# Performance work log

Measured on AMD Instinct MI355X. Metric: run time of the kernel, lower is better.

## Reference

```python
import jax, jax.numpy as jnp
from jax import lax
import numpy as np

NUM_SUBCNNS = 3      # num_classes - 1
C_FEAT = 1024        # backbone feature channels (hard-coded in CAM loop)
STRIDE = 32          # 224 -> 7 spatial reduction, like densenet121 features


def setup_inputs() -> dict:
    key = jax.random.key(0)
    ks = jax.random.split(key, 8)
    B, H, W = 32, 224, 224
    x = jax.random.normal(ks[0], (B, 3, H, W), dtype=jnp.float32)
    # Stand-in backbone per branch: conv 3->1024, kernel=stride=32 (same output
    # shape/dataflow as densenet121 features: [B,1024,7,7]).
    Wb = jax.random.normal(ks[1], (NUM_SUBCNNS, C_FEAT, 3, STRIDE, STRIDE), dtype=jnp.float32) * 0.02
    bb = jnp.zeros((NUM_SUBCNNS, C_FEAT), dtype=jnp.float32)
    # projection head: Linear(1024,512) -> ReLU -> (Dropout, eval=identity) -> Linear(512,2)
    p1_w = jax.random.normal(ks[2], (NUM_SUBCNNS, 512, C_FEAT), dtype=jnp.float32) * 0.02
    p1_b = jnp.zeros((NUM_SUBCNNS, 512), dtype=jnp.float32)
    p2_w = jax.random.normal(ks[3], (NUM_SUBCNNS, 2, 512), dtype=jnp.float32) * 0.02
    p2_b = jnp.zeros((NUM_SUBCNNS, 2), dtype=jnp.float32)
    # classifier Linear(1024,2): only its weight is used, for the CAM reduction
    cls_w = jax.random.normal(ks[4], (NUM_SUBCNNS, 2, C_FEAT), dtype=jnp.float32) * 0.02
    return {"x": x, "Wb": Wb, "bb": bb, "p1_w": p1_w, "p1_b": p1_b,
            "p2_w": p2_w, "p2_b": p2_b, "cls_w": cls_w}


def reference(x, Wb, bb, p1_w, p1_b, p2_w, p2_b, cls_w):
    ranking_outputs = []
    cam_outputs = []
    features_list = []
    for i in range(NUM_SUBCNNS):
        # backbone feature extraction: [B,3,224,224] -> [B,1024,7,7]
        feats = lax.conv_general_dilated(
            x, Wb[i], window_strides=(STRIDE, STRIDE), padding="VALID",
            dimension_numbers=("NCHW", "OIHW", "NCHW")) + bb[i][None, :, None, None]
        features_list.append(feats)
        # global average pool over H,W
        pooled = jnp.mean(feats, axis=(2, 3))                       # [B,1024]
        # projection MLP (dropout is identity at inference)
        h = jax.nn.relu(pooled @ p1_w[i].T + p1_b[i])               # [B,512]
        logits = h @ p2_w[i].T + p2_b[i]                            # [B,2]
        ranking_outputs.append(jax.nn.softmax(logits, axis=1)[:, 1:2])  # [B,1]
        # CAM: the torch double python-loop == one contraction over channels
        cam = jax.nn.relu(jnp.einsum("oc,bchw->obhw", cls_w[i], feats))  # [2,B,7,7]
        cam_outputs.append((cam[0], cam[1]))
    ranking = jnp.concatenate(ranking_outputs, axis=1)              # [B,3]
    return ranking, cam_outputs, features_list
```

## Files before the change

### kernel.cpp

```cpp
#include <hip/hip_runtime.h>
#include <hip/hip_bf16.h>
#include <math.h>

#define NSUB   3
#define CFEAT  1024
#define KDIM   3072
#define MDIM   1568
#define BATCH  32
#define NMT    25
#define NKT    96

#define OUT_CAM   96
#define OUT_FEAT  9504
#define FEAT_PER_BRANCH (BATCH * CFEAT * 49)

#define WS_A      0
#define WS_W      (9600 * 1024)
#define WS_POOLED (WS_W + 18432 * 1024)
#define WS_H      (WS_POOLED + NSUB * BATCH * CFEAT * 4)
#define WS_CAMP   (WS_H + NSUB * BATCH * 512 * 4)

typedef __attribute__((ext_vector_type(8))) short bf16x8;
typedef __attribute__((ext_vector_type(4))) float f32x4;

__device__ __forceinline__ short b16(float f){
    __hip_bfloat16 h = __float2bfloat16(f);
    return *reinterpret_cast<short*>(&h);
}
__device__ __forceinline__ bf16x8 pack8(float4 a, float4 b){
    bf16x8 r;
    r[0]=b16(a.x); r[1]=b16(a.y); r[2]=b16(a.z); r[3]=b16(a.w);
    r[4]=b16(b.x); r[5]=b16(b.y); r[6]=b16(b.z); r[7]=b16(b.w);
    return r;
}

__global__ __launch_bounds__(256) void prep_frag(
    const float* __restrict__ x, const float* __restrict__ w,
    bf16x8* __restrict__ Af, bf16x8* __restrict__ Wf)
{
    int bid = blockIdx.x, t = threadIdx.x;
    if (bid < 4608) {
        int g = bid * 256 + t;
        int chunk = g >> 6, l = g & 63;
        int ni = chunk & 3, KT = (chunk >> 2) % 96, NTg = chunk / 384;
        int n = NTg * 64 + ni * 16 + (l & 15);
        int k = KT * 32 + (l >> 4) * 8;
        const float* src = w + (size_t)n * KDIM + k;
        Wf[(size_t)chunk * 64 + l] = pack8(*(const float4*)src, *(const float4*)(src + 4));
    } else {
        int g = (bid - 4608) * 256 + t;
        int chunk = g >> 6, l = g & 63;
        int mi = chunk & 3, KT = (chunk >> 2) % 96, MT = chunk / 384;
        int m  = MT * 64 + mi * 16 + (l & 15);
        int k0 = KT * 32 + (l >> 4) * 8;
        bf16x8 v;
        if (m < MDIM) {
            int b = m / 49, p = m % 49, ph = p / 7, pw = p % 7;
            int ch = k0 >> 10, r = (k0 >> 5) & 31, s = k0 & 31;
            const float* src = x + (((size_t)(b*3 + ch)*224 + ph*32 + r)*224 + pw*32 + s);
            v = pack8(*(const float4*)src, *(const float4*)(src + 4));
        } else {
            v = (bf16x8){0,0,0,0,0,0,0,0};
        }
        Af[(size_t)chunk * 64 + l] = v;
    }
}

__global__ __launch_bounds__(128) void conv_mfma(
    const bf16x8* __restrict__ Af, const bf16x8* __restrict__ Wf,
    const float* __restrict__ bb, float* __restrict__ out)
{
    int bid = (int)blockIdx.x;
    bid = (bid & 7) * 75 + (bid >> 3);
    const int i   = bid / 200;
    const int rem = bid % 200;
    const int NTb = rem / 25, MT = rem % 25;

    const int wv = threadIdx.x >> 6, l = threadIdx.x & 63;
    const int NT = NTb + wv * 8;
    const int lrow = l & 15, q = l >> 4;

    const bf16x8* Ab = Af + (size_t)(MT * 384) * 64 + l;
    const bf16x8* Bb = Wf + (size_t)((i*16 + NT) * 384) * 64 + l;

    f32x4 acc[4][4] = {};
    bf16x8 fa0[4], fb0[4], fa1[4], fb1[4];

#pragma unroll
    for (int m = 0; m < 4; ++m) { fa0[m] = Ab[m*64]; fb0[m] = Bb[m*64]; }

    for (int KT = 0; KT < NKT; KT += 2) {
        {
            const bf16x8* An = Ab + (KT + 1) * 256;
            const bf16x8* Bn = Bb + (KT + 1) * 256;
#pragma unroll
            for (int m = 0; m < 4; ++m) { fa1[m] = An[m*64]; fb1[m] = Bn[m*64]; }
        }
#pragma unroll
        for (int mi = 0; mi < 4; ++mi)
#pragma unroll
            for (int ni = 0; ni < 4; ++ni)
                acc[mi][ni] = __builtin_amdgcn_mfma_f32_16x16x32_bf16(
                    fa0[mi], fb0[ni], acc[mi][ni], 0, 0, 0);
        if (KT + 2 < NKT) {
            const bf16x8* An = Ab + (KT + 2) * 256;
            const bf16x8* Bn = Bb + (KT + 2) * 256;
#pragma unroll
            for (int m = 0; m < 4; ++m) { fa0[m] = An[m*64]; fb0[m] = Bn[m*64]; }
        }
#pragma unroll
        for (int mi = 0; mi < 4; ++mi)
#pragma unroll
            for (int ni = 0; ni < 4; ++ni)
                acc[mi][ni] = __builtin_amdgcn_mfma_f32_16x16x32_bf16(
                    fa1[mi], fb1[ni], acc[mi][ni], 0, 0, 0);
    }

    float* featb = out + OUT_FEAT + (size_t)i * FEAT_PER_BRANCH;
    float bias[4];
#pragma unroll
    for (int ni = 0; ni < 4; ++ni)
        bias[ni] = bb[i*CFEAT + NT*64 + ni*16 + lrow];
#pragma unroll
    for (int mi = 0; mi < 4; ++mi) {
        int mbase = MT*64 + mi*16 + q*4;
#pragma unroll
        for (int rr = 0; rr < 4; ++rr) {
            int m = mbase + rr;
            if (m >= MDIM) continue;
            int b = m / 49, p = m % 49;
#pragma unroll
            for (int ni = 0; ni < 4; ++ni) {
                int n = NT*64 + ni*16 + lrow;
                featb[(size_t)(b*CFEAT + n)*49 + p] = acc[mi][ni][rr] + bias[ni];
            }
        }
    }
}

__global__ __launch_bounds__(128) void cam_pool(
    const float* __restrict__ feat, const float* __restrict__ cls_w,
    float* __restrict__ pooled, float* __restrict__ camp)
{
    __shared__ float fs[128][50];
    int bid = blockIdx.x;
    int i = bid >> 8, b = (bid >> 3) & 31, ch = bid & 7;
    int t = threadIdx.x;
    int c0 = ch * 128;
    const float* f = feat + ((size_t)(i*BATCH + b) * CFEAT + c0) * 49;

    for (int qq = 0; qq < 49; ++qq) {
        int e = qq*128 + t;
        fs[e / 49][e % 49] = f[e];
    }
    __syncthreads();

    {
        float s = 0.f;
#pragma unroll
        for (int k = 0; k < 49; ++k) s += fs[t][k];
        pooled[(size_t)(i*BATCH + b) * CFEAT + c0 + t] = s * (1.f/49.f);
    }

    if (t < 98) {
        int o = t / 49, p = t % 49;
        const float* w = cls_w + (size_t)i * 2 * CFEAT + o * CFEAT + c0;
        float s = 0.f;
        for (int c = 0; c < 128; ++c) s += w[c] * fs[c][p];
        camp[(size_t)bid * 98 + t] = s;
    }
}

__global__ __launch_bounds__(256) void mlp1_kernel(
    const float* __restrict__ pooled, const float* __restrict__ p1w,
    const float* __restrict__ p1b, float* __restrict__ h,
    const float* __restrict__ camp, float* __restrict__ out_cam)
{
    if (blockIdx.x >= 48) {
        int fid = (blockIdx.x - 48) * 256 + threadIdx.x;
        if (fid < NSUB * 2 * MDIM) {
            int io = fid / MDIM, rem = fid % MDIM;
            int b = rem / 49, p = rem % 49;
            int i = io >> 1, o = io & 1;
            float s = 0.f;
#pragma unroll
            for (int c = 0; c < 8; ++c)
                s += camp[(size_t)(((i*BATCH + b)*8) + c) * 98 + o*49 + p];
            out_cam[fid] = fmaxf(s, 0.f);
        }
        return;
    }
    __shared__ float ps[32 * 256];
    int i = blockIdx.x >> 4, jc = blockIdx.x & 15;
    int t = threadIdx.x;
    int j = jc*32 + (t & 31);
    int bg = (t >> 5) * 4;
    float acc[4] = {};
    const float* wrow = p1w + ((size_t)i*512 + j) * CFEAT;
    for (int kc = 0; kc < 4; ++kc) {
        __syncthreads();
#pragma unroll
        for (int qq = 0; qq < 8; ++qq) {
            int f4 = t + qq*256;
            int b = f4 >> 6, k4 = (f4 & 63) * 4;
            *(float4*)&ps[b*256 + k4] =
                *(const float4*)&pooled[((size_t)i*32 + b)*CFEAT + kc*256 + k4];
        }
        __syncthreads();
        const float* wk = wrow + kc*256;
        for (int k = 0; k < 256; k += 4) {
            float4 w4 = *(const float4*)(wk + k);
#pragma unroll
            for (int qq = 0; qq < 4; ++qq) {
                const float* pr = &ps[(bg + qq)*256 + k];
                acc[qq] += w4.x*pr[0] + w4.y*pr[1] + w4.z*pr[2] + w4.w*pr[3];
            }
        }
    }
    float bias = p1b[i*512 + j];
#pragma unroll
    for (int qq = 0; qq < 4; ++qq)
        h[((size_t)i*32 + bg + qq)*512 + j] = fmaxf(acc[qq] + bias, 0.f);
}

__global__ void mlp2_kernel(const float* __restrict__ h, const float* __restrict__ p2w,
                            const float* __restrict__ p2b, float* __restrict__ out)
{
    __shared__ float part[256];
    int i = blockIdx.x, t = threadIdx.x;
    int b = t & 31, kc = t >> 5;
    const float* hv = h + ((size_t)i*32 + b)*512 + kc*64;
    const float* w0 = p2w + (size_t)i*1024 + kc*64;
    const float* w1 = w0 + 512;
    float s = 0.f;
    for (int k = 0; k < 64; ++k) s += hv[k] * (w1[k] - w0[k]);
    part[t] = s;
    __syncthreads();
    if (t < 32) {
        float d = 0.f;
#pragma unroll
        for (int qq = 0; qq < 8; ++qq) d += part[qq*32 + t];
        d += p2b[i*2 + 1] - p2b[i*2 + 0];
        out[b*NSUB + i] = 1.f / (1.f + expf(-d));
    }
}

extern "C" void kernel_launch(void* const* d_in, const int* in_sizes, int n_in,
                              void* d_out, int out_size, void* d_ws, size_t ws_size,
                              hipStream_t stream)
{
    const float* x    = (const float*)d_in[0];
    const float* Wb   = (const float*)d_in[1];
    const float* bbp  = (const float*)d_in[2];
    const float* p1w  = (const float*)d_in[3];
    const float* p1b  = (const float*)d_in[4];
    const float* p2w  = (const float*)d_in[5];
    const float* p2b  = (const float*)d_in[6];
    const float* clsw = (const float*)d_in[7];
    float* out = (float*)d_out;

    char* ws = (char*)d_ws;
    bf16x8* Af    = (bf16x8*)(ws + WS_A);
    bf16x8* Wf    = (bf16x8*)(ws + WS_W);
    float* pooled = (float*)(ws + WS_POOLED);
    float* hbuf   = (float*)(ws + WS_H);
    float* camp   = (float*)(ws + WS_CAMP);

    prep_frag<<<4608 + 2400, 256, 0, stream>>>(x, Wb, Af, Wf);
    conv_mfma<<<600, 128, 0, stream>>>(Af, Wf, bbp, out);
    cam_pool<<<NSUB*BATCH*8, 128, 0, stream>>>(out + OUT_FEAT, clsw, pooled, camp);
    mlp1_kernel<<<48 + 37, 256, 0, stream>>>(pooled, p1w, p1b, hbuf, camp, out + OUT_CAM);
    mlp2_kernel<<<NSUB, 256, 0, stream>>>(hbuf, p2w, p2b, out);
}
```

Before: 122.0 us.

## Triple-buffer MFMA operand loads and stage conv epilogue through LDS

Replaces the two-deep register prefetch in the conv GEMM with a three-stage rotation (loads for k-tile kt+2 are issued before the MFMAs for kt), so more global loads are in flight while the matrix cores work. The epilogue now writes each wave's 64x64 accumulator tile into padded shared memory and then stores it with each lane owning one spatial row, so consecutive lanes write adjacent feature elements instead of scattering across channels. It also adds a min-blocks-per-SM launch bound of 2. The extra register buffers and about 33KB of LDS per block may limit occupancy, and since each wave only touches its own LDS slice no barrier is needed.

```diff
diff --git a/kernel.cpp b/kernel.cpp
--- a/kernel.cpp
+++ b/kernel.cpp
@@ -66,10 +66,12 @@
     }
 }
 
-__global__ __launch_bounds__(128) void conv_mfma(
+__global__ __launch_bounds__(128, 2) void conv_mfma(
     const bf16x8* __restrict__ Af, const bf16x8* __restrict__ Wf,
     const float* __restrict__ bb, float* __restrict__ out)
 {
+    __shared__ float eplds[2][64 * 65];
+
     int bid = (int)blockIdx.x;
     bid = (bid & 7) * 75 + (bid >> 3);
     const int i   = bid / 200;
@@ -84,57 +86,55 @@
     const bf16x8* Bb = Wf + (size_t)((i*16 + NT) * 384) * 64 + l;
 
     f32x4 acc[4][4] = {};
-    bf16x8 fa0[4], fb0[4], fa1[4], fb1[4];
-
-#pragma unroll
-    for (int m = 0; m < 4; ++m) { fa0[m] = Ab[m*64]; fb0[m] = Bb[m*64]; }
-
-    for (int KT = 0; KT < NKT; KT += 2) {
-        {
-            const bf16x8* An = Ab + (KT + 1) * 256;
-            const bf16x8* Bn = Bb + (KT + 1) * 256;
-#pragma unroll
-            for (int m = 0; m < 4; ++m) { fa1[m] = An[m*64]; fb1[m] = Bn[m*64]; }
-        }
+    bf16x8 a0[4], b0[4], a1[4], b1[4], a2[4], b2[4];
+
+    auto LOADT = [&](bf16x8 (&Ad)[4], bf16x8 (&Bd)[4], int KT){
+        const bf16x8* An = Ab + KT * 256;
+        const bf16x8* Bn = Bb + KT * 256;
+#pragma unroll
+        for (int m2 = 0; m2 < 4; ++m2) { Ad[m2] = An[m2*64]; Bd[m2] = Bn[m2*64]; }
+    };
+    auto MFMAT = [&](bf16x8 (&As)[4], bf16x8 (&Bs)[4]){
 #pragma unroll
         for (int mi = 0; mi < 4; ++mi)
 #pragma unroll
             for (int ni = 0; ni < 4; ++ni)
                 acc[mi][ni] = __builtin_amdgcn_mfma_f32_16x16x32_bf16(
-                    fa0[mi], fb0[ni], acc[mi][ni], 0, 0, 0);
-        if (KT + 2 < NKT) {
-            const bf16x8* An = Ab + (KT + 2) * 256;
-            const bf16x8* Bn = Bb + (KT + 2) * 256;
-#pragma unroll
-            for (int m = 0; m < 4; ++m) { fa0[m] = An[m*64]; fb0[m] = Bn[m*64]; }
-        }
-#pragma unroll
-        for (int mi = 0; mi < 4; ++mi)
-#pragma unroll
-            for (int ni = 0; ni < 4; ++ni)
-                acc[mi][ni] = __builtin_amdgcn_mfma_f32_16x16x32_bf16(
-                    fa1[mi], fb1[ni], acc[mi][ni], 0, 0, 0);
-    }
-
-    float* featb = out + OUT_FEAT + (size_t)i * FEAT_PER_BRANCH;
+                    As[mi], Bs[ni], acc[mi][ni], 0, 0, 0);
+    };
+
+    LOADT(a0, b0, 0);
+    LOADT(a1, b1, 1);
+    for (int kt = 0; kt < NKT; kt += 3) {
+        LOADT(a2, b2, kt + 2);
+        MFMAT(a0, b0);
+        if (kt + 3 < NKT) LOADT(a0, b0, kt + 3);
+        MFMAT(a1, b1);
+        if (kt + 4 < NKT) LOADT(a1, b1, kt + 4);
+        MFMAT(a2, b2);
+    }
+
     float bias[4];
 #pragma unroll
     for (int ni = 0; ni < 4; ++ni)
         bias[ni] = bb[i*CFEAT + NT*64 + ni*16 + lrow];
-#pragma unroll
-    for (int mi = 0; mi < 4; ++mi) {
-        int mbase = MT*64 + mi*16 + q*4;
-#pragma unroll
-        for (int rr = 0; rr < 4; ++rr) {
-            int m = mbase + rr;
-            if (m >= MDIM) continue;
-            int b = m / 49, p = m % 49;
-#pragma unroll
-            for (int ni = 0; ni < 4; ++ni) {
-                int n = NT*64 + ni*16 + lrow;
-                featb[(size_t)(b*CFEAT + n)*49 + p] = acc[mi][ni][rr] + bias[ni];
-            }
-        }
+    float* ep = eplds[wv];
+#pragma unroll
+    for (int mi = 0; mi < 4; ++mi)
+#pragma unroll
+        for (int ni = 0; ni < 4; ++ni)
+#pragma unroll
+            for (int rr = 0; rr < 4; ++rr)
+                ep[(mi*16 + q*4 + rr) * 65 + ni*16 + lrow] = acc[mi][ni][rr] + bias[ni];
+
+    float* featb = out + OUT_FEAT + (size_t)i * FEAT_PER_BRANCH;
+    int m = MT*64 + l;
+    if (m < MDIM) {
+        int b = m / 49, p = m % 49;
+        float* base = featb + (size_t)(b*CFEAT + NT*64) * 49 + p;
+#pragma unroll 8
+        for (int c = 0; c < 64; ++c)
+            base[c * 49] = ep[l*65 + c];
     }
 }
 
```

Result: faster. 109.6 us (-10.2%).

## Stage A tiles through double-buffered LDS with 128x64 block tiles in conv GEMM

Applied to the files above, without the earlier changes.

The conv GEMM now uses 256-thread blocks, each computing a 128x64 output tile with four waves arranged 2x2. A fragments are loaded straight into double-buffered LDS with global_load_lds, so the waves sharing an A tile read it once instead of each reading it from global memory. B fragments are prefetched into registers one step ahead, and the MFMA sections run at raised wave priority. This cuts redundant global loads of A, at the cost of block-wide barriers, extra LDS traffic and one padded M tile that reads past the A buffer into unused rows.

```diff
diff --git a/kernel.cpp b/kernel.cpp
--- a/kernel.cpp
+++ b/kernel.cpp
@@ -7,8 +7,7 @@
 #define KDIM   3072
 #define MDIM   1568
 #define BATCH  32
-#define NMT    25
-#define NKT    96
+#define NK     48
 
 #define OUT_CAM   96
 #define OUT_FEAT  9504
@@ -32,6 +31,12 @@
     r[0]=b16(a.x); r[1]=b16(a.y); r[2]=b16(a.z); r[3]=b16(a.w);
     r[4]=b16(b.x); r[5]=b16(b.y); r[6]=b16(b.z); r[7]=b16(b.w);
     return r;
+}
+
+typedef const __attribute__((address_space(1))) void* gas1_t;
+typedef __attribute__((address_space(3))) void* las3_t;
+__device__ __forceinline__ void gl_lds16(const short* g, char* l){
+    __builtin_amdgcn_global_load_lds((gas1_t)g, (las3_t)l, 16, 0, 0);
 }
 
 __global__ __launch_bounds__(256) void prep_frag(
@@ -66,73 +71,112 @@
     }
 }
 
-__global__ __launch_bounds__(128) void conv_mfma(
+__global__ __launch_bounds__(256, 3) void conv_mfma(
     const bf16x8* __restrict__ Af, const bf16x8* __restrict__ Wf,
     const float* __restrict__ bb, float* __restrict__ out)
 {
+    __shared__ __align__(16) char lds[32768];
+
     int bid = (int)blockIdx.x;
-    bid = (bid & 7) * 75 + (bid >> 3);
-    const int i   = bid / 200;
-    const int rem = bid % 200;
-    const int NTb = rem / 25, MT = rem % 25;
-
-    const int wv = threadIdx.x >> 6, l = threadIdx.x & 63;
-    const int NT = NTb + wv * 8;
-    const int lrow = l & 15, q = l >> 4;
-
-    const bf16x8* Ab = Af + (size_t)(MT * 384) * 64 + l;
-    const bf16x8* Bb = Wf + (size_t)((i*16 + NT) * 384) * 64 + l;
-
-    f32x4 acc[4][4] = {};
-    bf16x8 fa0[4], fb0[4], fa1[4], fb1[4];
-
-#pragma unroll
-    for (int m = 0; m < 4; ++m) { fa0[m] = Ab[m*64]; fb0[m] = Bb[m*64]; }
-
-    for (int KT = 0; KT < NKT; KT += 2) {
-        {
-            const bf16x8* An = Ab + (KT + 1) * 256;
-            const bf16x8* Bn = Bb + (KT + 1) * 256;
-#pragma unroll
-            for (int m = 0; m < 4; ++m) { fa1[m] = An[m*64]; fb1[m] = Bn[m*64]; }
-        }
-#pragma unroll
-        for (int mi = 0; mi < 4; ++mi)
-#pragma unroll
-            for (int ni = 0; ni < 4; ++ni)
-                acc[mi][ni] = __builtin_amdgcn_mfma_f32_16x16x32_bf16(
-                    fa0[mi], fb0[ni], acc[mi][ni], 0, 0, 0);
-        if (KT + 2 < NKT) {
-            const bf16x8* An = Ab + (KT + 2) * 256;
-            const bf16x8* Bn = Bb + (KT + 2) * 256;
-#pragma unroll
-            for (int m = 0; m < 4; ++m) { fa0[m] = An[m*64]; fb0[m] = Bn[m*64]; }
-        }
-#pragma unroll
-        for (int mi = 0; mi < 4; ++mi)
-#pragma unroll
-            for (int ni = 0; ni < 4; ++ni)
-                acc[mi][ni] = __builtin_amdgcn_mfma_f32_16x16x32_bf16(
-                    fa1[mi], fb1[ni], acc[mi][ni], 0, 0, 0);
+    bid = (bid & 7) * 78 + (bid >> 3);
+    const int i   = bid / 208;
+    const int rem = bid % 208;
+    const int nt  = rem / 13, mt = rem % 13;
+
+    const int t = threadIdx.x, wv = t >> 6, l = t & 63;
+    const int wr = wv >> 1, wc = wv & 1;
+    const int lrow = l & 15, lsl = l >> 4;
+
+    const bf16x8* Ag[4]; int Ad[4];
+#pragma unroll
+    for (int q = 0; q < 4; ++q) {
+        int chunk = (2*mt + (wv >> 1))*384 + (wv & 1)*4 + q;
+        Ag[q] = Af + (size_t)chunk * 64 + l;
+        Ad[q] = (wv*4 + q) * 1024;
+    }
+
+    const int NTg = i*16 + nt;
+    const bf16x8* Bp[2][2];
+#pragma unroll
+    for (int ni = 0; ni < 2; ++ni)
+#pragma unroll
+        for (int kk = 0; kk < 2; ++kk)
+            Bp[ni][kk] = Wf + (size_t)(NTg*384 + kk*4 + wc*2 + ni) * 64 + l;
+
+    f32x4 acc[4][2] = {};
+    bf16x8 bgA[2][2], bgB[2][2];
+
+#pragma unroll
+    for (int q = 0; q < 4; ++q) gl_lds16((const short*)Ag[q], lds + Ad[q]);
+#pragma unroll
+    for (int ni = 0; ni < 2; ++ni)
+#pragma unroll
+        for (int kk = 0; kk < 2; ++kk)
+            bgA[ni][kk] = *Bp[ni][kk];
+
+    auto COMPUTE = [&](const char* base, bf16x8 (&BG)[2][2]) {
+        bf16x8 af[4][2];
+#pragma unroll
+        for (int kk = 0; kk < 2; ++kk)
+#pragma unroll
+            for (int mi = 0; mi < 4; ++mi)
+                af[mi][kk] = *(const bf16x8*)(base + ((wr*2 + kk)*4 + mi)*1024 + l*16);
+        __builtin_amdgcn_s_setprio(1);
+#pragma unroll
+        for (int kk = 0; kk < 2; ++kk)
+#pragma unroll
+            for (int mi = 0; mi < 4; ++mi)
+#pragma unroll
+                for (int ni = 0; ni < 2; ++ni)
+                    acc[mi][ni] = __builtin_amdgcn_mfma_f32_16x16x32_bf16(
+                        af[mi][kk], BG[ni][kk], acc[mi][ni], 0, 0, 0);
+        __builtin_amdgcn_s_setprio(0);
+    };
+
+    for (int kt = 0; kt < NK; kt += 2) {
+        __syncthreads();
+        if (kt + 1 < NK) {
+#pragma unroll
+            for (int q = 0; q < 4; ++q)
+                gl_lds16((const short*)(Ag[q] + (kt+1)*512), lds + 16384 + Ad[q]);
+#pragma unroll
+            for (int ni = 0; ni < 2; ++ni)
+#pragma unroll
+                for (int kk = 0; kk < 2; ++kk)
+                    bgB[ni][kk] = Bp[ni][kk][(size_t)(kt+1)*512];
+        }
+        COMPUTE(lds, bgA);
+        __syncthreads();
+        if (kt + 2 < NK) {
+#pragma unroll
+            for (int q = 0; q < 4; ++q)
+                gl_lds16((const short*)(Ag[q] + (kt+2)*512), lds + Ad[q]);
+#pragma unroll
+            for (int ni = 0; ni < 2; ++ni)
+#pragma unroll
+                for (int kk = 0; kk < 2; ++kk)
+                    bgA[ni][kk] = Bp[ni][kk][(size_t)(kt+2)*512];
+        }
+        COMPUTE(lds + 16384, bgB);
     }
 
     float* featb = out + OUT_FEAT + (size_t)i * FEAT_PER_BRANCH;
-    float bias[4];
-#pragma unroll
-    for (int ni = 0; ni < 4; ++ni)
-        bias[ni] = bb[i*CFEAT + NT*64 + ni*16 + lrow];
+    float bias[2];
+#pragma unroll
+    for (int ni = 0; ni < 2; ++ni)
+        bias[ni] = bb[i*CFEAT + nt*64 + wc*32 + ni*16 + lrow];
 #pragma unroll
     for (int mi = 0; mi < 4; ++mi) {
-        int mbase = MT*64 + mi*16 + q*4;
-#pragma unroll
-        for (int rr = 0; rr < 4; ++rr) {
-            int m = mbase + rr;
+        int mbase = mt*128 + wr*64 + mi*16 + lsl*4;
+#pragma unroll
+        for (int r = 0; r < 4; ++r) {
+            int m = mbase + r;
             if (m >= MDIM) continue;
-            int b = m / 49, p = m % 49;
-#pragma unroll
-            for (int ni = 0; ni < 4; ++ni) {
-                int n = NT*64 + ni*16 + lrow;
-                featb[(size_t)(b*CFEAT + n)*49 + p] = acc[mi][ni][rr] + bias[ni];
+            int b = m/49, p = m%49;
+#pragma unroll
+            for (int ni = 0; ni < 2; ++ni) {
+                int n = nt*64 + wc*32 + ni*16 + lrow;
+                featb[(size_t)(b*CFEAT + n)*49 + p] = acc[mi][ni][r] + bias[ni];
             }
         }
     }
@@ -267,7 +311,7 @@
     float* camp   = (float*)(ws + WS_CAMP);
 
     prep_frag<<<4608 + 2400, 256, 0, stream>>>(x, Wb, Af, Wf);
-    conv_mfma<<<600, 128, 0, stream>>>(Af, Wf, bbp, out);
+    conv_mfma<<<624, 256, 0, stream>>>(Af, Wf, bbp, out);
     cam_pool<<<NSUB*BATCH*8, 128, 0, stream>>>(out + OUT_FEAT, clsw, pooled, camp);
     mlp1_kernel<<<48 + 37, 256, 0, stream>>>(pooled, p1w, p1b, hbuf, camp, out + OUT_CAM);
     mlp2_kernel<<<NSUB, 256, 0, stream>>>(hbuf, p2w, p2b, out);
```

New measurement: 117.5 us. 1.04x faster.
